# Kernel optimization log

Hardware: AMD Instinct MI355X
Metric: run time of the kernel (lower is better)

The kernel has to match this reference:

```python
import jax, jax.numpy as jnp
import numpy as np

B, S, D = 2, 2048, 2048
H, HKV, HD = 16, 4, 128
GROUPS = H // HKV
SCALE = HD ** -0.5
ROPE_THETA = 10000.0
NEG = -1e9


def _rope_cos_sin():
    inv_freq = 1.0 / (ROPE_THETA ** (jnp.arange(0, HD, 2, dtype=jnp.float32) / HD))  # [HD/2]
    pos = jnp.arange(S, dtype=jnp.float32)
    freqs = pos[:, None] * inv_freq[None, :]            # [S, HD/2]
    emb = jnp.concatenate([freqs, freqs], axis=-1)      # [S, HD]
    cos = jnp.broadcast_to(jnp.cos(emb)[None], (B, S, HD))
    sin = jnp.broadcast_to(jnp.sin(emb)[None], (B, S, HD))
    return cos, sin


def setup_inputs() -> dict:
    key = jax.random.key(0)
    ks = jax.random.split(key, 5)
    hidden_states = jax.random.normal(ks[0], (B, S, D), dtype=jnp.float32)
    cos, sin = _rope_cos_sin()
    causal = jnp.where(jnp.arange(S)[:, None] >= jnp.arange(S)[None, :], 0.0, NEG).astype(jnp.float32)
    attn_mask = jnp.broadcast_to(causal[None, None], (B, 1, S, S))
    wq = jax.random.normal(ks[1], (H * HD, D), dtype=jnp.float32) * (D ** -0.5)
    wk = jax.random.normal(ks[2], (HKV * HD, D), dtype=jnp.float32) * (D ** -0.5)
    wv = jax.random.normal(ks[3], (HKV * HD, D), dtype=jnp.float32) * (D ** -0.5)
    wo = jax.random.normal(ks[4], (D, H * HD), dtype=jnp.float32) * (D ** -0.5)
    return {"hidden_states": hidden_states, "cos": cos, "sin": sin,
            "attn_mask": attn_mask, "wq": wq, "wk": wk, "wv": wv, "wo": wo}


def _rotate_half(x):
    x1, x2 = x[..., : HD // 2], x[..., HD // 2:]
    return jnp.concatenate([-x2, x1], axis=-1)


def reference(hidden_states, cos, sin, attn_mask, wq, wk, wv, wo):
    # projections (torch Linear: x @ W.T), reshape to [B, heads, S, HD]
    q = (hidden_states @ wq.T).reshape(B, S, H, HD).transpose(0, 2, 1, 3)
    k = (hidden_states @ wk.T).reshape(B, S, HKV, HD).transpose(0, 2, 1, 3)
    v = (hidden_states @ wv.T).reshape(B, S, HKV, HD).transpose(0, 2, 1, 3)
    # RoPE (cos/sin broadcast over head dim)
    c = cos[:, None, :, :]
    s = sin[:, None, :, :]
    q = q * c + _rotate_half(q) * s
    k = k * c + _rotate_half(k) * s
    # GQA: repeat each kv head GROUPS times consecutively (matches repeat_kv)
    k = jnp.repeat(k, GROUPS, axis=1)
    v = jnp.repeat(v, GROUPS, axis=1)
    logits = jnp.einsum('bhqd,bhkd->bhqk', q, k) * SCALE + attn_mask
    w = jax.nn.softmax(logits.astype(jnp.float32), axis=-1).astype(q.dtype)
    out = jnp.einsum('bhqk,bhkd->bhqd', w, v)            # [B,H,S,HD]
    out = out.transpose(0, 2, 1, 3).reshape(B, S, H * HD)
    return out @ wo.T
```

## Files before the change

### kernel.cpp

```cpp
#include <hip/hip_runtime.h>

typedef __attribute__((ext_vector_type(8))) short bf16x8;
typedef __attribute__((ext_vector_type(4))) float f32x4;
typedef __attribute__((ext_vector_type(16))) float f32x16;
typedef __attribute__((ext_vector_type(8))) unsigned short u16x8;
typedef __attribute__((ext_vector_type(4))) unsigned u32x4;
typedef unsigned short u16;

#define GLOBAL_AS __attribute__((address_space(1)))
#define LDS_AS __attribute__((address_space(3)))

#define S_ 2048
#define SMK_ 0.12751741406106783f

static __device__ __forceinline__ u16 f2bf(float f) {
  unsigned u = __builtin_bit_cast(unsigned, f);
  u += 0x7fffu + ((u >> 16) & 1u);
  return (u16)(u >> 16);
}
static __device__ __forceinline__ float bf2f(u16 h) {
  return __builtin_bit_cast(float, ((unsigned)h) << 16);
}
static __device__ __forceinline__ float exp2_raw(float x) {
  float r; asm("v_exp_f32 %0, %1" : "=v"(r) : "v"(x)); return r;
}
static __device__ __forceinline__ unsigned cvtpk(float lo, float hi_) {
  unsigned r; asm("v_cvt_pk_bf16_f32 %0, %1, %2" : "=v"(r) : "v"(lo), "v"(hi_)); return r;
}
static __device__ __forceinline__ float tmax16(const f32x16& s) {
  float a0 = fmaxf(s[0], s[1]),  a1 = fmaxf(s[2], s[3]);
  float a2 = fmaxf(s[4], s[5]),  a3 = fmaxf(s[6], s[7]);
  float a4 = fmaxf(s[8], s[9]),  a5 = fmaxf(s[10], s[11]);
  float a6 = fmaxf(s[12], s[13]), a7 = fmaxf(s[14], s[15]);
  return fmaxf(fmaxf(fmaxf(a0, a1), fmaxf(a2, a3)),
               fmaxf(fmaxf(a4, a5), fmaxf(a6, a7)));
}
static __device__ __forceinline__ float tsum16(const f32x16& s) {
  float a0 = s[0] + s[1],  a1 = s[2] + s[3];
  float a2 = s[4] + s[5],  a3 = s[6] + s[7];
  float a4 = s[8] + s[9],  a5 = s[10] + s[11];
  float a6 = s[12] + s[13], a7 = s[14] + s[15];
  return ((a0 + a1) + (a2 + a3)) + ((a4 + a5) + (a6 + a7));
}

__global__ __launch_bounds__(256)
void cvt_all(const float* __restrict__ h, const float* __restrict__ wq,
             const float* __restrict__ wk, const float* __restrict__ wv,
             const float* __restrict__ wo, u16* __restrict__ Xbf,
             u16* __restrict__ Wqkv, u16* __restrict__ Wo) {
  const int bid = blockIdx.x;
  const float* src; u16* dst; long base;
  if (bid < 4096)      { src = h;  dst = Xbf;            base = (long)bid * 2048; }
  else if (bid < 6144) { src = wq; dst = Wqkv;           base = (long)(bid - 4096) * 2048; }
  else if (bid < 6656) { src = wk; dst = Wqkv + 4194304; base = (long)(bid - 6144) * 2048; }
  else if (bid < 7168) { src = wv; dst = Wqkv + 5242880; base = (long)(bid - 6656) * 2048; }
  else                 { src = wo; dst = Wo;             base = (long)(bid - 7168) * 2048; }
  const long i = base + (long)threadIdx.x * 8;
  f32x4 a = *(const f32x4*)(src + i);
  f32x4 b = *(const f32x4*)(src + i + 4);
  u16x8 o;
  o[0] = f2bf(a[0]); o[1] = f2bf(a[1]); o[2] = f2bf(a[2]); o[3] = f2bf(a[3]);
  o[4] = f2bf(b[0]); o[5] = f2bf(b[1]); o[6] = f2bf(b[2]); o[7] = f2bf(b[3]);
  *(u16x8*)(dst + i) = o;
}

template <int NJ, bool BF16OUT>
__global__ __launch_bounds__(512, 2)
void gemm256(const u16* __restrict__ A, const u16* __restrict__ Bw,
             void* __restrict__ Cp, int M, int N, int K) {
  __shared__ u16 LA[4][2][4096];
  __shared__ u16 LB[4][NJ / 2][4096];

  const int tid = threadIdx.x;
  const int wave = tid >> 6, lane = tid & 63;
  const int fr = lane & 15, fg = lane >> 4;
  const int wm = (wave >> 2) * 128;
  const int wn = (wave & 3) * (NJ * 16);
  const long rowA = (long)blockIdx.y * 256;
  const long rowB = (long)blockIdx.x * (NJ * 64);

  const int srow = tid >> 2;
  const int sc8 = (tid & 3) ^ (srow & 3);
  const int wbase = wave * 512;

  const int nt = K >> 5;

  f32x4 acc[8][NJ] = {};

#define STAGE_A(pt)                                                          \
  {                                                                          \
    const int _b = (pt) & 3;                                                 \
    const long _k = (long)(pt) * 32 + sc8 * 8;                               \
    __builtin_amdgcn_global_load_lds(                                        \
        (GLOBAL_AS void*)(A + (rowA + srow) * K + _k),                       \
        (LDS_AS void*)(&LA[_b][0][wbase]), 16, 0, 0);                        \
    __builtin_amdgcn_global_load_lds(                                        \
        (GLOBAL_AS void*)(A + (rowA + 128 + srow) * K + _k),                 \
        (LDS_AS void*)(&LA[_b][1][wbase]), 16, 0, 0);                        \
  }
#define STAGE_B(pt)                                                          \
  {                                                                          \
    const int _b = (pt) & 3;                                                 \
    const long _k = (long)(pt) * 32 + sc8 * 8;                               \
    __builtin_amdgcn_global_load_lds(                                        \
        (GLOBAL_AS void*)(Bw + (rowB + srow) * K + _k),                      \
        (LDS_AS void*)(&LB[_b][0][wbase]), 16, 0, 0);                        \
    if (NJ == 4)                                                             \
      __builtin_amdgcn_global_load_lds(                                      \
          (GLOBAL_AS void*)(Bw + (rowB + 128 + srow) * K + _k),              \
          (LDS_AS void*)(&LB[_b][NJ / 2 - 1][wbase]), 16, 0, 0);             \
  }

  STAGE_A(0); STAGE_B(0);
  STAGE_A(1); STAGE_B(1);
  STAGE_A(2); STAGE_B(2);

  for (int t = 0; t < nt; ++t) {
    const int rem = nt - 1 - t;
    if (NJ == 4) {
      if (rem >= 2)      asm volatile("s_waitcnt vmcnt(8)" ::: "memory");
      else if (rem == 1) asm volatile("s_waitcnt vmcnt(4)" ::: "memory");
      else               asm volatile("s_waitcnt vmcnt(0)" ::: "memory");
    } else {
      if (rem >= 2)      asm volatile("s_waitcnt vmcnt(6)" ::: "memory");
      else if (rem == 1) asm volatile("s_waitcnt vmcnt(3)" ::: "memory");
      else               asm volatile("s_waitcnt vmcnt(0)" ::: "memory");
    }
    __builtin_amdgcn_s_barrier();

    const u16* Ah = LA[t & 3][wm >> 7];
    const u16* Bh = LB[t & 3][NJ == 4 ? (wn >> 7) : 0];
    const bool pf = (t + 3) < nt;

    bf16x8 af0[4], bfv[NJ];
#pragma unroll
    for (int mi = 0; mi < 4; ++mi) {
      const int rl = mi * 16 + fr;
      af0[mi] = *(const bf16x8*)&Ah[rl * 32 + ((fg ^ (rl & 3)) << 3)];
    }
#pragma unroll
    for (int nj = 0; nj < NJ; ++nj) {
      const int rb = (wn & 127) + nj * 16 + fr;
      bfv[nj] = *(const bf16x8*)&Bh[rb * 32 + ((fg ^ (rb & 3)) << 3)];
    }
    if (pf) STAGE_A(t + 3);
    __builtin_amdgcn_s_setprio(1);
#pragma unroll
    for (int mi = 0; mi < 4; ++mi)
#pragma unroll
      for (int nj = 0; nj < NJ; ++nj)
        acc[mi][nj] = __builtin_amdgcn_mfma_f32_16x16x32_bf16(af0[mi], bfv[nj], acc[mi][nj], 0, 0, 0);
    __builtin_amdgcn_s_setprio(0);

    bf16x8 af1[4];
#pragma unroll
    for (int mi = 0; mi < 4; ++mi) {
      const int rl = 64 + mi * 16 + fr;
      af1[mi] = *(const bf16x8*)&Ah[rl * 32 + ((fg ^ (rl & 3)) << 3)];
    }
    if (pf) STAGE_B(t + 3);
    __builtin_amdgcn_s_setprio(1);
#pragma unroll
    for (int mi = 0; mi < 4; ++mi)
#pragma unroll
      for (int nj = 0; nj < NJ; ++nj)
        acc[4 + mi][nj] = __builtin_amdgcn_mfma_f32_16x16x32_bf16(af1[mi], bfv[nj], acc[4 + mi][nj], 0, 0, 0);
    __builtin_amdgcn_s_setprio(0);

    __builtin_amdgcn_s_barrier();
  }
#undef STAGE_A
#undef STAGE_B

#pragma unroll
  for (int mi = 0; mi < 8; ++mi)
#pragma unroll
    for (int nj = 0; nj < NJ; ++nj)
#pragma unroll
      for (int r = 0; r < 4; ++r) {
        const long row = rowA + wm + mi * 16 + fg * 4 + r;
        const long col = rowB + wn + nj * 16 + fr;
        if (BF16OUT) ((u16*)Cp)[row * N + col] = f2bf(acc[mi][nj][r]);
        else         ((float*)Cp)[row * N + col] = acc[mi][nj][r];
      }
}

__global__ __launch_bounds__(256)
void rope_rearrange(const u16* __restrict__ QKV, const float* __restrict__ cosb,
                    const float* __restrict__ sinb, u16* __restrict__ Qr,
                    u16* __restrict__ Kr) {
  const int m = blockIdx.x;
  const int b = m >> 11, s = m & 2047;
  const int t = threadIdx.x;
  const u16* row = QKV + (long)m * 3072;
  const float* cp = cosb + (long)m * 128;
  const float* sp = sinb + (long)m * 128;
#pragma unroll
  for (int i = 0; i < 4; ++i) {
    const int idx = i * 256 + t;
    const int h = idx >> 6, d = idx & 63;
    const float x1 = bf2f(row[h * 128 + d]);
    const float x2 = bf2f(row[h * 128 + d + 64]);
    const float c = cp[d], sv = sp[d];
    const long o = ((long)(b * 16 + h) * S_ + s) * 128 + d;
    Qr[o] = f2bf(x1 * c - x2 * sv);
    Qr[o + 64] = f2bf(x2 * c + x1 * sv);
  }
  {
    const int h = t >> 6, d = t & 63;
    const float x1 = bf2f(row[2048 + h * 128 + d]);
    const float x2 = bf2f(row[2048 + h * 128 + d + 64]);
    const float c = cp[d], sv = sp[d];
    const long o = ((long)(b * 4 + h) * S_ + s) * 128 + d;
    Kr[o] = f2bf((x1 * c - x2 * sv) * SMK_);
    Kr[o + 64] = f2bf((x2 * c + x1 * sv) * SMK_);
  }
}

__global__ __launch_bounds__(256)
void transpose_v(const u16* __restrict__ QKV, u16* __restrict__ Vt) {
  __shared__ u16 t[32][33];
  const int s0 = blockIdx.x * 32, d0 = blockIdx.y * 32;
  const int bk = blockIdx.z;
  const int b = bk >> 2, kh = bk & 3;
  const int tx = threadIdx.x & 31, ty = threadIdx.x >> 5;
  const u16* src = QKV + 2560 + (long)kh * 128;
#pragma unroll
  for (int i = 0; i < 4; ++i) {
    const int sl = ty + i * 8;
    t[sl][tx] = src[(long)(b * S_ + s0 + sl) * 3072 + d0 + tx];
  }
  __syncthreads();
  u16* dst = Vt + (long)(b * 4 + kh) * 128 * S_;
#pragma unroll
  for (int i = 0; i < 4; ++i) {
    const int dl = ty + i * 8;
    dst[(long)(d0 + dl) * S_ + s0 + tx] = t[tx][dl];
  }
}

struct PA2 { bf16x8 a, b; };
static __device__ __forceinline__ PA2 pack_half(const f32x16 s) {
  PA2 out;
#pragma unroll
  for (int ks2 = 0; ks2 < 2; ++ks2) {
    const int rb = ks2 * 8;
    unsigned w0 = cvtpk(s[rb + 0], s[rb + 1]);
    unsigned w1 = cvtpk(s[rb + 2], s[rb + 3]);
    unsigned w2 = cvtpk(s[rb + 4], s[rb + 5]);
    unsigned w3 = cvtpk(s[rb + 6], s[rb + 7]);
    asm("v_permlane32_swap_b32 %0, %1" : "+v"(w0), "+v"(w2));
    asm("v_permlane32_swap_b32 %0, %1" : "+v"(w1), "+v"(w3));
    u32x4 pw; pw[0] = w0; pw[1] = w1; pw[2] = w2; pw[3] = w3;
    if (ks2 == 0) out.a = __builtin_bit_cast(bf16x8, pw);
    else          out.b = __builtin_bit_cast(bf16x8, pw);
  }
  return out;
}

template <int NH>
static __device__ __forceinline__ void attn_tile(
    const u16* __restrict__ Ks, const u16* __restrict__ Vs,
    const bf16x8 (&qf)[8], f32x16 (&acc)[4], float& m_run, float& l_run,
    const int kv0, const int qwmin, const int qg, const int l31,
    const int hi, const int r7) {
  f32x16 s[NH];
#pragma unroll
  for (int hh = 0; hh < NH; ++hh) s[hh] = (f32x16){};
  __builtin_amdgcn_s_setprio(1);
#pragma unroll
  for (int ds = 0; ds < 8; ++ds) {
    const int ch = ((2 * ds + hi) ^ r7) << 3;
#pragma unroll
    for (int hh = 0; hh < NH; ++hh) {
      const bf16x8 ka = *(const bf16x8*)&Ks[(hh * 32 + l31) * 128 + ch];
      s[hh] = __builtin_amdgcn_mfma_f32_32x32x16_bf16(ka, qf[ds], s[hh], 0, 0, 0);
    }
  }
  __builtin_amdgcn_s_setprio(0);

  if (kv0 + NH * 32 - 1 > qwmin) {
#pragma unroll
    for (int hh = 0; hh < NH; ++hh)
#pragma unroll
      for (int r = 0; r < 16; ++r) {
        const int cr = (r & 3) + 8 * (r >> 2) + 4 * hi;
        if (kv0 + hh * 32 + cr > qg) s[hh][r] = -3.0e38f;
      }
  }

  float mx = tmax16(s[0]);
  if (NH == 2) mx = fmaxf(mx, tmax16(s[1]));
  mx = fmaxf(mx, __shfl_xor(mx, 32));

  if (__any(mx > m_run + 8.0f)) {
    const float mn = fmaxf(m_run, mx);
    const float scq = exp2_raw(m_run - mn);
    m_run = mn; l_run *= scq;
#pragma unroll
    for (int r = 0; r < 16; ++r) {
      const int cr = (r & 3) + 8 * (r >> 2) + 4 * hi;
      const float sr = __shfl(scq, cr);
      acc[0][r] *= sr; acc[1][r] *= sr; acc[2][r] *= sr; acc[3][r] *= sr;
    }
  }

#pragma unroll
  for (int hh = 0; hh < NH; ++hh)
#pragma unroll
    for (int r = 0; r < 16; ++r) s[hh][r] = exp2_raw(s[hh][r] - m_run);
  float rs = tsum16(s[0]);
  if (NH == 2) rs += tsum16(s[1]);
  rs += __shfl_xor(rs, 32);
  l_run += rs;

  bf16x8 pa[2 * NH];
#pragma unroll
  for (int hh = 0; hh < NH; ++hh) {
    const PA2 p = pack_half(s[hh]);
    pa[2 * hh] = p.a; pa[2 * hh + 1] = p.b;
  }
  __builtin_amdgcn_s_setprio(1);
#pragma unroll
  for (int nj = 0; nj < 4; ++nj) {
    const int vrow = (nj * 32 + l31) * 64;
#pragma unroll
    for (int ks = 0; ks < 2 * NH; ++ks) {
      const bf16x8 vf = *(const bf16x8*)&Vs[vrow + (((2 * ks + hi) ^ r7) << 3)];
      acc[nj] = __builtin_amdgcn_mfma_f32_32x32x16_bf16(pa[ks], vf, acc[nj], 0, 0, 0);
    }
  }
  __builtin_amdgcn_s_setprio(0);
}

#define PAIRS_PER_GRP 64u
__global__ __launch_bounds__(256)
void attn_fwd(const u16* __restrict__ Qr, const u16* __restrict__ Kr,
              const u16* __restrict__ Vt, u16* __restrict__ Att,
              unsigned* __restrict__ ctrs) {
  __shared__ u16 Ks[64 * 128];
  __shared__ u16 Vs[128 * 64];
  __shared__ unsigned s_uid;

  const int tid = threadIdx.x, wave = tid >> 6, lane = tid & 63;
  const int l31 = lane & 31, hi = lane >> 5, r7 = lane & 7;

  const int xcc = __builtin_amdgcn_s_getreg(6164) & 7;

  for (;;) {
    __syncthreads();
    if (tid == 0) {
      unsigned got = 0xffffffffu;
#pragma unroll
      for (int k = 0; k < 8; ++k) {
        const int sq = (xcc + k) & 7;
        const unsigned v = atomicAdd(&ctrs[sq], 1u);
        if (v < PAIRS_PER_GRP) { got = (unsigned)sq * PAIRS_PER_GRP + v; break; }
      }
      s_uid = got;
    }
    __syncthreads();
    const unsigned uid = s_uid;
    if (uid == 0xffffffffu) break;

    const int g = uid >> 6;
    const int u = uid & 63;
    const int qt = 31 - (u >> 1);
    const int hp = u & 1;
    const int b = g >> 2, kh = g & 3;
    const int h = kh * 4 + hp * 2 + (wave >> 1);
    const int qwmin = qt * 64 + (wave & 1) * 32;

    const u16* Qb = Qr + (long)(b * 16 + h) * S_ * 128;
    const u16* Kb = Kr + (long)(b * 4 + kh) * S_ * 128;
    const u16* Vg = Vt + (long)(b * 4 + kh) * 128 * (long)S_;

    bf16x8 qf[8];
    const u16* qrow = Qb + (long)(qwmin + l31) * 128 + hi * 8;
#pragma unroll
    for (int ds = 0; ds < 8; ++ds) qf[ds] = *(const bf16x8*)(qrow + ds * 16);

    f32x16 acc[4] = {};
    float m_run = -1e30f, l_run = 0.f;
    const int qg = qwmin + l31;

    const int ntiles = qt + 1;
    for (int t = 0; t < ntiles; ++t) {
      const int kv0 = t * 64;
      __syncthreads();
#pragma unroll
      for (int c = 0; c < 4; ++c) {
        const int slab = wave * 4 + c;
        const int offu = slab * 512 + lane * 8;
        const int kvl = offu >> 7;
        const int kc = ((offu >> 3) & 15) ^ (kvl & 7);
        __builtin_amdgcn_global_load_lds(
            (GLOBAL_AS void*)(Kb + (long)(kv0 + kvl) * 128 + kc * 8),
            (LDS_AS void*)(Ks + slab * 512), 16, 0, 0);
        const int dr = offu >> 6;
        const int vc = ((offu >> 3) & 7) ^ (dr & 7);
        __builtin_amdgcn_global_load_lds(
            (GLOBAL_AS void*)(Vg + (long)dr * S_ + kv0 + vc * 8),
            (LDS_AS void*)(Vs + slab * 512), 16, 0, 0);
      }
      __syncthreads();

      if (kv0 + 32 <= qwmin + 31)
        attn_tile<2>(Ks, Vs, qf, acc, m_run, l_run, kv0, qwmin, qg, l31, hi, r7);
      else if (kv0 <= qwmin + 31)
        attn_tile<1>(Ks, Vs, qf, acc, m_run, l_run, kv0, qwmin, qg, l31, hi, r7);
    }

    const float inv = 1.0f / l_run;
#pragma unroll
    for (int r = 0; r < 16; ++r) {
      const int cr = (r & 3) + 8 * (r >> 2) + 4 * hi;
      const float ir = __shfl(inv, cr);
      const long orow = ((long)b * S_ + qwmin + cr) * 2048 + h * 128 + l31;
      Att[orow]      = f2bf(acc[0][r] * ir);
      Att[orow + 32] = f2bf(acc[1][r] * ir);
      Att[orow + 64] = f2bf(acc[2][r] * ir);
      Att[orow + 96] = f2bf(acc[3][r] * ir);
    }
  }
}

extern "C" void kernel_launch(void* const* d_in, const int* in_sizes, int n_in,
                              void* d_out, int out_size, void* d_ws, size_t ws_size,
                              hipStream_t stream) {
  const float* hidden = (const float*)d_in[0];
  const float* cosb = (const float*)d_in[1];
  const float* sinb = (const float*)d_in[2];
  const float* wq = (const float*)d_in[4];
  const float* wk = (const float*)d_in[5];
  const float* wv = (const float*)d_in[6];
  const float* wo = (const float*)d_in[7];
  float* out = (float*)d_out;

  u16* Xbf  = (u16*)d_ws;
  u16* Wqkv = Xbf + 8388608;
  u16* Wo   = Wqkv + 6291456;
  u16* QKV  = Wo + 4194304;
  u16* Qr   = QKV + 12582912;
  u16* Kr   = Qr + 8388608;
  u16* Vtp  = Kr + 2097152;
  u16* Att  = Xbf;
  if (ws_size < (size_t)44040192 * 2) return;

  cvt_all<<<dim3(9216), dim3(256), 0, stream>>>(hidden, wq, wk, wv, wo, Xbf, Wqkv, Wo);
  gemm256<4, true><<<dim3(12, 16), dim3(512), 0, stream>>>(Xbf, Wqkv, (void*)QKV, 4096, 3072, 2048);
  rope_rearrange<<<dim3(4096), dim3(256), 0, stream>>>(QKV, cosb, sinb, Qr, Kr);
  transpose_v<<<dim3(64, 4, 8), dim3(256), 0, stream>>>(QKV, Vtp);
  hipMemsetAsync((void*)Wqkv, 0, 32, stream);
  attn_fwd<<<dim3(512), dim3(256), 0, stream>>>(Qr, Kr, Vtp, Att, (unsigned*)Wqkv);
  gemm256<2, false><<<dim3(16, 16), dim3(512), 0, stream>>>(Att, Wo, (void*)out, 4096, 2048, 2048);
}
```

Measured before the change: 257.4 us.

## Double-buffer K/V tiles in attention with async prefetch two tiles ahead

```diff
diff --git a/kernel.cpp b/kernel.cpp
--- a/kernel.cpp
+++ b/kernel.cpp
@@ -338,14 +338,33 @@
 void attn_fwd(const u16* __restrict__ Qr, const u16* __restrict__ Kr,
               const u16* __restrict__ Vt, u16* __restrict__ Att,
               unsigned* __restrict__ ctrs) {
-  __shared__ u16 Ks[64 * 128];
-  __shared__ u16 Vs[128 * 64];
+  __shared__ u16 Ks[2][64 * 128];
+  __shared__ u16 Vs[2][128 * 64];
   __shared__ unsigned s_uid;
 
   const int tid = threadIdx.x, wave = tid >> 6, lane = tid & 63;
   const int l31 = lane & 31, hi = lane >> 5, r7 = lane & 7;
 
   const int xcc = __builtin_amdgcn_s_getreg(6164) & 7;
+
+#define STAGE_KV(tt)                                                          \
+  {                                                                           \
+    const int _bi = (tt) & 1;                                                 \
+    _Pragma("unroll") for (int c = 0; c < 4; ++c) {                           \
+      const int slab = wave * 4 + c;                                          \
+      const int offu = slab * 512 + lane * 8;                                 \
+      const int kvl = offu >> 7;                                              \
+      const int kc = ((offu >> 3) & 15) ^ (kvl & 7);                          \
+      __builtin_amdgcn_global_load_lds(                                       \
+          (GLOBAL_AS void*)(Kb + (long)((tt) * 64 + kvl) * 128 + kc * 8),     \
+          (LDS_AS void*)(Ks[_bi] + slab * 512), 16, 0, 0);                    \
+      const int dr = offu >> 6;                                               \
+      const int vc = ((offu >> 3) & 7) ^ (dr & 7);                            \
+      __builtin_amdgcn_global_load_lds(                                       \
+          (GLOBAL_AS void*)(Vg + (long)dr * S_ + (tt) * 64 + vc * 8),         \
+          (LDS_AS void*)(Vs[_bi] + slab * 512), 16, 0, 0);                    \
+    }                                                                         \
+  }
 
   for (;;) {
     __syncthreads();
@@ -384,31 +403,25 @@
     float m_run = -1e30f, l_run = 0.f;
     const int qg = qwmin + l31;
 
-    const int ntiles = qt + 1;
-    for (int t = 0; t < ntiles; ++t) {
+    const int nt = qt + 1;
+    STAGE_KV(0);
+    if (nt > 1) STAGE_KV(1);
+
+    for (int t = 0; t < nt; ++t) {
       const int kv0 = t * 64;
-      __syncthreads();
-#pragma unroll
-      for (int c = 0; c < 4; ++c) {
-        const int slab = wave * 4 + c;
-        const int offu = slab * 512 + lane * 8;
-        const int kvl = offu >> 7;
-        const int kc = ((offu >> 3) & 15) ^ (kvl & 7);
-        __builtin_amdgcn_global_load_lds(
-            (GLOBAL_AS void*)(Kb + (long)(kv0 + kvl) * 128 + kc * 8),
-            (LDS_AS void*)(Ks + slab * 512), 16, 0, 0);
-        const int dr = offu >> 6;
-        const int vc = ((offu >> 3) & 7) ^ (dr & 7);
-        __builtin_amdgcn_global_load_lds(
-            (GLOBAL_AS void*)(Vg + (long)dr * S_ + kv0 + vc * 8),
-            (LDS_AS void*)(Vs + slab * 512), 16, 0, 0);
-      }
-      __syncthreads();
+      if (t == nt - 1) asm volatile("s_waitcnt vmcnt(0)" ::: "memory");
+      else             asm volatile("s_waitcnt vmcnt(8)" ::: "memory");
+      __builtin_amdgcn_s_barrier();
 
       if (kv0 + 32 <= qwmin + 31)
-        attn_tile<2>(Ks, Vs, qf, acc, m_run, l_run, kv0, qwmin, qg, l31, hi, r7);
-      else if (kv0 <= qwmin + 31)
-        attn_tile<1>(Ks, Vs, qf, acc, m_run, l_run, kv0, qwmin, qg, l31, hi, r7);
+        attn_tile<2>(Ks[t & 1], Vs[t & 1], qf, acc, m_run, l_run, kv0, qwmin, qg, l31, hi, r7);
+      else
+        attn_tile<1>(Ks[t & 1], Vs[t & 1], qf, acc, m_run, l_run, kv0, qwmin, qg, l31, hi, r7);
+
+      __builtin_amdgcn_sched_barrier(0);
+      asm volatile("s_waitcnt lgkmcnt(0)" ::: "memory");
+      __builtin_amdgcn_s_barrier();
+      if (t + 2 < nt) STAGE_KV(t + 2);
     }
 
     const float inv = 1.0f / l_run;
@@ -423,6 +436,7 @@
       Att[orow + 96] = f2bf(acc[3][r] * ir);
     }
   }
+#undef STAGE_KV
 }
 
 extern "C" void kernel_launch(void* const* d_in, const int* in_sizes, int n_in,
```

After: 257.8 us. About the same (+0.2%).
